# Kernel tuning notes

Measured on AMD Instinct MI355X. Metric: run time of the kernel, lower is better.

## Reference

```python
import jax, jax.numpy as jnp
import numpy as np

C = 2048
N = 8
K = C // N  # 256
B = 4096


def setup_inputs() -> dict:
    key = jax.random.key(0)
    ks = jax.random.split(key, 9)
    s_in = 1.0 / np.sqrt(C)
    s_k = 1.0 / np.sqrt(K)
    return {
        "x": jax.random.normal(ks[0], (B, C), dtype=jnp.float32),
        # weights stored [in, out] (y = x @ W + b), equivalent to torch Linear
        "W_theta": jax.random.uniform(ks[1], (C, K), jnp.float32, -s_in, s_in),
        "b_theta": jax.random.uniform(ks[2], (K,), jnp.float32, -s_in, s_in),
        "W_phi": jax.random.uniform(ks[3], (C, K), jnp.float32, -s_in, s_in),
        "b_phi": jax.random.uniform(ks[4], (K,), jnp.float32, -s_in, s_in),
        "W_f": jax.random.uniform(ks[5], (C, K), jnp.float32, -s_in, s_in),
        "b_f": jax.random.uniform(ks[6], (K,), jnp.float32, -s_in, s_in),
        "W_g": jax.random.uniform(ks[7], (K, C), jnp.float32, -s_k, s_k),
        "b_g": jax.random.uniform(ks[8], (C,), jnp.float32, -s_k, s_k),
    }


def reference(x, W_theta, b_theta, W_phi, b_phi, W_f, b_f, W_g, b_g):
    theta = x @ W_theta + b_theta          # [B, K]
    phi = x @ W_phi + b_phi                # [B, K]
    f = x @ W_f + b_f                      # [B, K]
    # outer product per sample -> [B, K, K], softmax over last dim
    scores = jax.nn.softmax(theta[:, :, None] * phi[:, None, :], axis=-1)
    t = jnp.einsum('bij,bj->bi', scores, f)  # [B, K]
    return x + t @ W_g + b_g               # residual, [B, C]
```

## Files before the change

kernel.cpp:

```cpp
#include <hip/hip_runtime.h>

constexpr int Bsz   = 4096;
constexpr int Cdim  = 2048;
constexpr int Kdim  = 256;
constexpr int PROJW = 3 * Kdim;

typedef __attribute__((ext_vector_type(8))) short short8;
typedef __attribute__((ext_vector_type(4))) float floatx4;

__device__ __forceinline__ unsigned short f2bf(float f) {
    unsigned int u = __float_as_uint(f);
    u += 0x7FFFu + ((u >> 16) & 1u);
    return (unsigned short)(u >> 16);
}

__device__ __forceinline__ void load16(const void* g, void* lds) {
    __builtin_amdgcn_global_load_lds(
        (const __attribute__((address_space(1))) unsigned int*)g,
        (__attribute__((address_space(3))) unsigned int*)lds, 16, 0, 0);
}

__global__ __launch_bounds__(256) void cast_x_kernel(
    const float* __restrict__ in, unsigned short* __restrict__ out)
{
    const int i = blockIdx.x * 256 + threadIdx.x;
    float4 v = reinterpret_cast<const float4*>(in)[i];
    ushort4 o;
    o.x = f2bf(v.x); o.y = f2bf(v.y); o.z = f2bf(v.z); o.w = f2bf(v.w);
    reinterpret_cast<ushort4*>(out)[i] = o;
}

__global__ __launch_bounds__(256) void transpose_all(
    const float* __restrict__ Wt, const float* __restrict__ Wp,
    const float* __restrict__ Wf, const float* __restrict__ Wg,
    unsigned short* __restrict__ Wcat, unsigned short* __restrict__ WgT)
{
    __shared__ float tile[32][33];
    const int z = blockIdx.y;
    const float* __restrict__ in;
    unsigned short* __restrict__ out;
    int R, C;
    if (z < 3) {
        in = (z == 0) ? Wt : (z == 1) ? Wp : Wf;
        out = Wcat + (size_t)z * Kdim * Cdim;
        R = Cdim; C = Kdim;
    } else {
        in = Wg; out = WgT; R = Kdim; C = Cdim;
    }
    const int ctiles = C / 32;
    const int c0 = (blockIdx.x % ctiles) * 32;
    const int r0 = (blockIdx.x / ctiles) * 32;
    const int tx = threadIdx.x & 31, ty = threadIdx.x >> 5;
#pragma unroll
    for (int i = ty; i < 32; i += 8)
        tile[i][tx] = in[(size_t)(r0 + i) * C + c0 + tx];
    __syncthreads();
#pragma unroll
    for (int i = ty; i < 32; i += 8)
        out[(size_t)(c0 + i) * R + r0 + tx] = f2bf(tile[tx][i]);
}

__global__ __launch_bounds__(256) void proj_mfma(
    const unsigned short* __restrict__ xb,
    const unsigned short* __restrict__ Wcat,
    const float* __restrict__ bt, const float* __restrict__ bp,
    const float* __restrict__ bff,
    float* __restrict__ proj)
{
    __shared__ short As[128 * 32];
    __shared__ short Bs[64 * 32];

    const int tid  = threadIdx.x;
    const int lane = tid & 63;
    const int wid  = tid >> 6;
    const int wr   = wid >> 1, wc = wid & 1;
    const int rowBase = blockIdx.x * 128;
    const int colBase = blockIdx.y * 64;
    const int w = colBase >> 8;
    const float* __restrict__ bias = (w == 0) ? bt : (w == 1) ? bp : bff;

    floatx4 acc[4][2] = {};

    const unsigned short* gA0;
    const unsigned short* gA1;
    {
        int c0 = tid, c1 = 256 + tid;
        gA0 = xb + (size_t)(rowBase + (c0 >> 2)) * Cdim + (c0 & 3) * 8;
        gA1 = xb + (size_t)(rowBase + (c1 >> 2)) * Cdim + (c1 & 3) * 8;
    }
    const unsigned short* gB =
        Wcat + (size_t)(colBase + (tid >> 2)) * Cdim + (tid & 3) * 8;

    short* ldsA0 = As + ((tid & ~63)) * 8;
    short* ldsA1 = As + (256 + (tid & ~63)) * 8;
    short* ldsB  = Bs + ((tid & ~63)) * 8;

    const int mrow = lane & 15;
    const int kgrp = lane >> 4;

    for (int kt = 0; kt < Cdim; kt += 32) {
        load16(gA0, ldsA0);
        load16(gA1, ldsA1);
        load16(gB,  ldsB);
        gA0 += 32; gA1 += 32; gB += 32;
        __syncthreads();

        short8 af[4], bfr[2];
#pragma unroll
        for (int i = 0; i < 4; ++i)
            af[i] = *(const short8*)&As[(wr * 64 + i * 16 + mrow) * 32 + kgrp * 8];
#pragma unroll
        for (int j = 0; j < 2; ++j)
            bfr[j] = *(const short8*)&Bs[(wc * 32 + j * 16 + mrow) * 32 + kgrp * 8];
#pragma unroll
        for (int i = 0; i < 4; ++i)
#pragma unroll
            for (int j = 0; j < 2; ++j)
                acc[i][j] = __builtin_amdgcn_mfma_f32_16x16x32_bf16(
                    af[i], bfr[j], acc[i][j], 0, 0, 0);
        __syncthreads();
    }

#pragma unroll
    for (int j = 0; j < 2; ++j) {
        const int col = colBase + wc * 32 + j * 16 + mrow;
        const float bv = bias[col & 255];
#pragma unroll
        for (int i = 0; i < 4; ++i) {
#pragma unroll
            for (int r = 0; r < 4; ++r) {
                const int row = rowBase + wr * 64 + i * 16 + kgrp * 4 + r;
                proj[(size_t)row * PROJW + col] = acc[i][j][r] + bv;
            }
        }
    }
}

__global__ __launch_bounds__(256) void attn_kernel(
    const float* __restrict__ proj, unsigned short* __restrict__ t)
{
    __shared__ float2 spf[4][Kdim];

    const int tid = threadIdx.x;
    const int s   = tid >> 6;
    const int l   = tid & 63;
    const int b   = blockIdx.x * 4 + s;
    const float* __restrict__ row = proj + (size_t)b * PROJW;

    float tl[4];
#pragma unroll
    for (int i = 0; i < 4; ++i) {
        const int j = l + i * 64;
        tl[i] = row[j] * 1.44269504f;
        spf[s][j] = make_float2(row[Kdim + j], row[2 * Kdim + j]);
    }
    __syncthreads();

    float2 sa[4] = {}, na[4] = {};
    const float2* __restrict__ sp = spf[s];
#pragma unroll 4
    for (int k = 0; k < Kdim; k += 2) {
        const float4 v = *reinterpret_cast<const float4*>(&sp[k]);
#pragma unroll
        for (int i = 0; i < 4; ++i) {
            const float e0 = __builtin_amdgcn_exp2f(tl[i] * v.x);
            const float e1 = __builtin_amdgcn_exp2f(tl[i] * v.z);
            sa[i].x += e0;
            sa[i].y += e1;
            na[i].x = fmaf(e0, v.y, na[i].x);
            na[i].y = fmaf(e1, v.w, na[i].y);
        }
    }
#pragma unroll
    for (int i = 0; i < 4; ++i) {
        const int j = l + i * 64;
        t[(size_t)b * Kdim + j] = f2bf((na[i].x + na[i].y) / (sa[i].x + sa[i].y));
    }
}

__global__ __launch_bounds__(256) void out_mfma(
    const unsigned short* __restrict__ tb,
    const unsigned short* __restrict__ WgT,
    const float* __restrict__ bg,
    const float* __restrict__ x,
    float* __restrict__ out)
{
    __shared__ short As[128 * 32];
    __shared__ short Bs[128 * 32];

    const int tid  = threadIdx.x;
    const int lane = tid & 63;
    const int wid  = tid >> 6;
    const int wr   = wid >> 1, wc = wid & 1;
    const int rowBase = blockIdx.x * 128;
    const int colBase = blockIdx.y * 128;

    floatx4 acc[4][4] = {};

    const unsigned short* gA0;
    const unsigned short* gA1;
    const unsigned short* gB0;
    const unsigned short* gB1;
    {
        int c0 = tid, c1 = 256 + tid;
        gA0 = tb  + (size_t)(rowBase + (c0 >> 2)) * Kdim + (c0 & 3) * 8;
        gA1 = tb  + (size_t)(rowBase + (c1 >> 2)) * Kdim + (c1 & 3) * 8;
        gB0 = WgT + (size_t)(colBase + (c0 >> 2)) * Kdim + (c0 & 3) * 8;
        gB1 = WgT + (size_t)(colBase + (c1 >> 2)) * Kdim + (c1 & 3) * 8;
    }
    short* ldsA0 = As + ((tid & ~63)) * 8;
    short* ldsA1 = As + (256 + (tid & ~63)) * 8;
    short* ldsB0 = Bs + ((tid & ~63)) * 8;
    short* ldsB1 = Bs + (256 + (tid & ~63)) * 8;

    const int mrow = lane & 15;
    const int kgrp = lane >> 4;

    for (int kt = 0; kt < Kdim; kt += 32) {
        load16(gA0, ldsA0); load16(gA1, ldsA1);
        load16(gB0, ldsB0); load16(gB1, ldsB1);
        gA0 += 32; gA1 += 32; gB0 += 32; gB1 += 32;
        __syncthreads();

        short8 af[4], bfr[4];
#pragma unroll
        for (int i = 0; i < 4; ++i)
            af[i]  = *(const short8*)&As[(wr * 64 + i * 16 + mrow) * 32 + kgrp * 8];
#pragma unroll
        for (int j = 0; j < 4; ++j)
            bfr[j] = *(const short8*)&Bs[(wc * 64 + j * 16 + mrow) * 32 + kgrp * 8];
#pragma unroll
        for (int i = 0; i < 4; ++i)
#pragma unroll
            for (int j = 0; j < 4; ++j)
                acc[i][j] = __builtin_amdgcn_mfma_f32_16x16x32_bf16(
                    af[i], bfr[j], acc[i][j], 0, 0, 0);
        __syncthreads();
    }

#pragma unroll
    for (int j = 0; j < 4; ++j) {
        const int col = colBase + wc * 64 + j * 16 + mrow;
        const float bv = bg[col];
#pragma unroll
        for (int i = 0; i < 4; ++i) {
#pragma unroll
            for (int r = 0; r < 4; ++r) {
                const int row = rowBase + wr * 64 + i * 16 + kgrp * 4 + r;
                out[(size_t)row * Cdim + col] =
                    acc[i][j][r] + bv + x[(size_t)row * Cdim + col];
            }
        }
    }
}

extern "C" void kernel_launch(void* const* d_in, const int* in_sizes, int n_in,
                              void* d_out, int out_size, void* d_ws, size_t ws_size,
                              hipStream_t stream) {
    const float* x  = (const float*)d_in[0];
    const float* Wt = (const float*)d_in[1];
    const float* bt = (const float*)d_in[2];
    const float* Wp = (const float*)d_in[3];
    const float* bp = (const float*)d_in[4];
    const float* Wf = (const float*)d_in[5];
    const float* bf = (const float*)d_in[6];
    const float* Wg = (const float*)d_in[7];
    const float* bg = (const float*)d_in[8];
    float* out = (float*)d_out;

    char* w = (char*)d_ws;
    float*          proj = (float*)w;
    unsigned short* xb   = (unsigned short*)(w + 12582912);
    unsigned short* Wcat = (unsigned short*)(w + 29360128);
    unsigned short* WgT  = (unsigned short*)(w + 32505856);
    unsigned short* tb   = (unsigned short*)(w + 33554432);

    cast_x_kernel<<<(Bsz * Cdim / 4) / 256, 256, 0, stream>>>(x, xb);
    transpose_all<<<dim3(512, 4), 256, 0, stream>>>(Wt, Wp, Wf, Wg, Wcat, WgT);
    proj_mfma<<<dim3(Bsz / 128, PROJW / 64), 256, 0, stream>>>(xb, Wcat, bt, bp, bf, proj);
    attn_kernel<<<Bsz / 4, 256, 0, stream>>>(proj, tb);
    out_mfma<<<dim3(Bsz / 128, Cdim / 128), 256, 0, stream>>>(tb, WgT, bg, x, out);
}
```

Baseline: 186.2 us.

## Split-K projection GEMM with 128x128 tiles, fuse prep kernels, reduce in attention

```diff
diff --git a/kernel.cpp b/kernel.cpp
--- a/kernel.cpp
+++ b/kernel.cpp
@@ -4,6 +4,7 @@
 constexpr int Cdim  = 2048;
 constexpr int Kdim  = 256;
 constexpr int PROJW = 3 * Kdim;
+constexpr int KSPLIT = 4;
 
 typedef __attribute__((ext_vector_type(8))) short short8;
 typedef __attribute__((ext_vector_type(4))) float floatx4;
@@ -20,23 +21,25 @@
         (__attribute__((address_space(3))) unsigned int*)lds, 16, 0, 0);
 }
 
-__global__ __launch_bounds__(256) void cast_x_kernel(
-    const float* __restrict__ in, unsigned short* __restrict__ out)
-{
-    const int i = blockIdx.x * 256 + threadIdx.x;
-    float4 v = reinterpret_cast<const float4*>(in)[i];
-    ushort4 o;
-    o.x = f2bf(v.x); o.y = f2bf(v.y); o.z = f2bf(v.z); o.w = f2bf(v.w);
-    reinterpret_cast<ushort4*>(out)[i] = o;
-}
-
-__global__ __launch_bounds__(256) void transpose_all(
+__global__ __launch_bounds__(256) void prep_kernel(
+    const float* __restrict__ x, unsigned short* __restrict__ xb,
     const float* __restrict__ Wt, const float* __restrict__ Wp,
     const float* __restrict__ Wf, const float* __restrict__ Wg,
     unsigned short* __restrict__ Wcat, unsigned short* __restrict__ WgT)
 {
     __shared__ float tile[32][33];
-    const int z = blockIdx.y;
+    const int bid = blockIdx.x;
+    if (bid < 8192) {
+        const int i = bid * 256 + threadIdx.x;
+        float4 v = reinterpret_cast<const float4*>(x)[i];
+        ushort4 o;
+        o.x = f2bf(v.x); o.y = f2bf(v.y); o.z = f2bf(v.z); o.w = f2bf(v.w);
+        reinterpret_cast<ushort4*>(xb)[i] = o;
+        return;
+    }
+    const int q = bid - 8192;
+    const int z = q >> 9;
+    const int tileId = q & 511;
     const float* __restrict__ in;
     unsigned short* __restrict__ out;
     int R, C;
@@ -48,8 +51,8 @@
         in = Wg; out = WgT; R = Kdim; C = Cdim;
     }
     const int ctiles = C / 32;
-    const int c0 = (blockIdx.x % ctiles) * 32;
-    const int r0 = (blockIdx.x / ctiles) * 32;
+    const int c0 = (tileId % ctiles) * 32;
+    const int r0 = (tileId / ctiles) * 32;
     const int tx = threadIdx.x & 31, ty = threadIdx.x >> 5;
 #pragma unroll
     for (int i = ty; i < 32; i += 8)
@@ -63,81 +66,76 @@
 __global__ __launch_bounds__(256) void proj_mfma(
     const unsigned short* __restrict__ xb,
     const unsigned short* __restrict__ Wcat,
-    const float* __restrict__ bt, const float* __restrict__ bp,
-    const float* __restrict__ bff,
-    float* __restrict__ proj)
+    float* __restrict__ pp)
 {
     __shared__ short As[128 * 32];
-    __shared__ short Bs[64 * 32];
+    __shared__ short Bs[128 * 32];
 
     const int tid  = threadIdx.x;
     const int lane = tid & 63;
     const int wid  = tid >> 6;
     const int wr   = wid >> 1, wc = wid & 1;
     const int rowBase = blockIdx.x * 128;
-    const int colBase = blockIdx.y * 64;
-    const int w = colBase >> 8;
-    const float* __restrict__ bias = (w == 0) ? bt : (w == 1) ? bp : bff;
-
-    floatx4 acc[4][2] = {};
-
-    const unsigned short* gA0;
-    const unsigned short* gA1;
-    {
-        int c0 = tid, c1 = 256 + tid;
-        gA0 = xb + (size_t)(rowBase + (c0 >> 2)) * Cdim + (c0 & 3) * 8;
-        gA1 = xb + (size_t)(rowBase + (c1 >> 2)) * Cdim + (c1 & 3) * 8;
-    }
-    const unsigned short* gB =
-        Wcat + (size_t)(colBase + (tid >> 2)) * Cdim + (tid & 3) * 8;
+    const int colBase = blockIdx.y * 128;
+    const int k0      = blockIdx.z * (Cdim / KSPLIT);
+
+    floatx4 acc[4][4] = {};
+
+    const unsigned short* gA0 = xb   + (size_t)(rowBase + (tid >> 2)) * Cdim + k0 + (tid & 3) * 8;
+    const unsigned short* gA1 = xb   + (size_t)(rowBase + 64 + (tid >> 2)) * Cdim + k0 + (tid & 3) * 8;
+    const unsigned short* gB0 = Wcat + (size_t)(colBase + (tid >> 2)) * Cdim + k0 + (tid & 3) * 8;
+    const unsigned short* gB1 = Wcat + (size_t)(colBase + 64 + (tid >> 2)) * Cdim + k0 + (tid & 3) * 8;
 
     short* ldsA0 = As + ((tid & ~63)) * 8;
     short* ldsA1 = As + (256 + (tid & ~63)) * 8;
-    short* ldsB  = Bs + ((tid & ~63)) * 8;
+    short* ldsB0 = Bs + ((tid & ~63)) * 8;
+    short* ldsB1 = Bs + (256 + (tid & ~63)) * 8;
 
     const int mrow = lane & 15;
     const int kgrp = lane >> 4;
 
-    for (int kt = 0; kt < Cdim; kt += 32) {
-        load16(gA0, ldsA0);
-        load16(gA1, ldsA1);
-        load16(gB,  ldsB);
-        gA0 += 32; gA1 += 32; gB += 32;
-        __syncthreads();
-
-        short8 af[4], bfr[2];
-#pragma unroll
-        for (int i = 0; i < 4; ++i)
-            af[i] = *(const short8*)&As[(wr * 64 + i * 16 + mrow) * 32 + kgrp * 8];
-#pragma unroll
-        for (int j = 0; j < 2; ++j)
-            bfr[j] = *(const short8*)&Bs[(wc * 32 + j * 16 + mrow) * 32 + kgrp * 8];
-#pragma unroll
-        for (int i = 0; i < 4; ++i)
-#pragma unroll
-            for (int j = 0; j < 2; ++j)
+    for (int kt = 0; kt < Cdim / KSPLIT; kt += 32) {
+        load16(gA0, ldsA0); load16(gA1, ldsA1);
+        load16(gB0, ldsB0); load16(gB1, ldsB1);
+        gA0 += 32; gA1 += 32; gB0 += 32; gB1 += 32;
+        __syncthreads();
+
+        short8 af[4], bfr[4];
+#pragma unroll
+        for (int i = 0; i < 4; ++i)
+            af[i]  = *(const short8*)&As[(wr * 64 + i * 16 + mrow) * 32 + kgrp * 8];
+#pragma unroll
+        for (int j = 0; j < 4; ++j)
+            bfr[j] = *(const short8*)&Bs[(wc * 64 + j * 16 + mrow) * 32 + kgrp * 8];
+#pragma unroll
+        for (int i = 0; i < 4; ++i)
+#pragma unroll
+            for (int j = 0; j < 4; ++j)
                 acc[i][j] = __builtin_amdgcn_mfma_f32_16x16x32_bf16(
                     af[i], bfr[j], acc[i][j], 0, 0, 0);
         __syncthreads();
     }
 
-#pragma unroll
-    for (int j = 0; j < 2; ++j) {
-        const int col = colBase + wc * 32 + j * 16 + mrow;
-        const float bv = bias[col & 255];
+    float* __restrict__ dst = pp + (size_t)blockIdx.z * Bsz * PROJW;
+#pragma unroll
+    for (int j = 0; j < 4; ++j) {
+        const int col = colBase + wc * 64 + j * 16 + mrow;
 #pragma unroll
         for (int i = 0; i < 4; ++i) {
 #pragma unroll
             for (int r = 0; r < 4; ++r) {
                 const int row = rowBase + wr * 64 + i * 16 + kgrp * 4 + r;
-                proj[(size_t)row * PROJW + col] = acc[i][j][r] + bv;
+                dst[(size_t)row * PROJW + col] = acc[i][j][r];
             }
         }
     }
 }
 
 __global__ __launch_bounds__(256) void attn_kernel(
-    const float* __restrict__ proj, unsigned short* __restrict__ t)
+    const float* __restrict__ pp,
+    const float* __restrict__ bt, const float* __restrict__ bp,
+    const float* __restrict__ bff,
+    unsigned short* __restrict__ t)
 {
     __shared__ float2 spf[4][Kdim];
 
@@ -145,14 +143,22 @@
     const int s   = tid >> 6;
     const int l   = tid & 63;
     const int b   = blockIdx.x * 4 + s;
-    const float* __restrict__ row = proj + (size_t)b * PROJW;
+    const size_t rowOff = (size_t)b * PROJW;
 
     float tl[4];
 #pragma unroll
     for (int i = 0; i < 4; ++i) {
         const int j = l + i * 64;
-        tl[i] = row[j] * 1.44269504f;
-        spf[s][j] = make_float2(row[Kdim + j], row[2 * Kdim + j]);
+        float th = bt[j], ph = bp[j], fv = bff[j];
+#pragma unroll
+        for (int z = 0; z < KSPLIT; ++z) {
+            const float* __restrict__ r = pp + (size_t)z * Bsz * PROJW + rowOff;
+            th += r[j];
+            ph += r[Kdim + j];
+            fv += r[2 * Kdim + j];
+        }
+        tl[i] = th * 1.44269504f;
+        spf[s][j] = make_float2(ph, fv);
     }
     __syncthreads();
 
@@ -197,17 +203,11 @@
 
     floatx4 acc[4][4] = {};
 
-    const unsigned short* gA0;
-    const unsigned short* gA1;
-    const unsigned short* gB0;
-    const unsigned short* gB1;
-    {
-        int c0 = tid, c1 = 256 + tid;
-        gA0 = tb  + (size_t)(rowBase + (c0 >> 2)) * Kdim + (c0 & 3) * 8;
-        gA1 = tb  + (size_t)(rowBase + (c1 >> 2)) * Kdim + (c1 & 3) * 8;
-        gB0 = WgT + (size_t)(colBase + (c0 >> 2)) * Kdim + (c0 & 3) * 8;
-        gB1 = WgT + (size_t)(colBase + (c1 >> 2)) * Kdim + (c1 & 3) * 8;
-    }
+    const unsigned short* gA0 = tb  + (size_t)(rowBase + (tid >> 2)) * Kdim + (tid & 3) * 8;
+    const unsigned short* gA1 = tb  + (size_t)(rowBase + 64 + (tid >> 2)) * Kdim + (tid & 3) * 8;
+    const unsigned short* gB0 = WgT + (size_t)(colBase + (tid >> 2)) * Kdim + (tid & 3) * 8;
+    const unsigned short* gB1 = WgT + (size_t)(colBase + 64 + (tid >> 2)) * Kdim + (tid & 3) * 8;
+
     short* ldsA0 = As + ((tid & ~63)) * 8;
     short* ldsA1 = As + (256 + (tid & ~63)) * 8;
     short* ldsB0 = Bs + ((tid & ~63)) * 8;
@@ -269,15 +269,14 @@
     float* out = (float*)d_out;
 
     char* w = (char*)d_ws;
-    float*          proj = (float*)w;
-    unsigned short* xb   = (unsigned short*)(w + 12582912);
-    unsigned short* Wcat = (unsigned short*)(w + 29360128);
-    unsigned short* WgT  = (unsigned short*)(w + 32505856);
-    unsigned short* tb   = (unsigned short*)(w + 33554432);
-
-    cast_x_kernel<<<(Bsz * Cdim / 4) / 256, 256, 0, stream>>>(x, xb);
-    transpose_all<<<dim3(512, 4), 256, 0, stream>>>(Wt, Wp, Wf, Wg, Wcat, WgT);
-    proj_mfma<<<dim3(Bsz / 128, PROJW / 64), 256, 0, stream>>>(xb, Wcat, bt, bp, bf, proj);
-    attn_kernel<<<Bsz / 4, 256, 0, stream>>>(proj, tb);
+    float*          pp   = (float*)w;
+    unsigned short* xb   = (unsigned short*)(w + 50331648);
+    unsigned short* Wcat = (unsigned short*)(w + 67108864);
+    unsigned short* WgT  = (unsigned short*)(w + 70254592);
+    unsigned short* tb   = (unsigned short*)(w + 71303168);
+
+    prep_kernel<<<10240, 256, 0, stream>>>(x, xb, Wt, Wp, Wf, Wg, Wcat, WgT);
+    proj_mfma<<<dim3(Bsz / 128, PROJW / 128, KSPLIT), 256, 0, stream>>>(xb, Wcat, pp);
+    attn_kernel<<<Bsz / 4, 256, 0, stream>>>(pp, bt, bp, bf, tb);
     out_mfma<<<dim3(Bsz / 128, Cdim / 128), 256, 0, stream>>>(tb, WgT, bg, x, out);
 }
```

After: 179.9 us. 1.03x faster.
